# Performance work log

Measured on AMD Instinct MI355X. Metric: run time of the kernel, lower is better.

## Reference

```python
import jax, jax.numpy as jnp
import numpy as np

B, N = 8, 48
NEMBED, EMBED_DIM, HID_DIM = 1000, 32, 32
IN_DIM = EMBED_DIM + 1  # feature dim after concatenating xfeat
N_OPS = 8  # exchangeable 3-tensor basis: identity + means over each nonempty axis subset


def setup_inputs() -> dict:
    key = jax.random.key(0)
    k1, k2, k3, k4, k5 = jax.random.split(key, 5)
    xcat = jax.random.randint(k1, (B, N), 0, NEMBED)
    xfeat = jax.random.normal(k2, (B, N), dtype=jnp.float32)
    embed_table = jax.random.normal(k3, (NEMBED, EMBED_DIM), dtype=jnp.float32)
    # SetEq3to3 coefficients: (in_dim, n_basis_ops, out_dim), Glorot-ish scale
    coefs = jax.random.normal(k4, (IN_DIM, N_OPS, HID_DIM), dtype=jnp.float32) * np.sqrt(2.0 / (IN_DIM + HID_DIM))
    eq_bias = jnp.zeros((HID_DIM,), dtype=jnp.float32)
    out_w = jax.random.normal(k5, (HID_DIM, 1), dtype=jnp.float32) * np.sqrt(1.0 / HID_DIM)
    out_b = jnp.zeros((1,), dtype=jnp.float32)
    return {"xcat": xcat, "xfeat": xfeat, "embed_table": embed_table,
            "coefs": coefs, "eq_bias": eq_bias, "out_w": out_w, "out_b": out_b}


def _set_eq3to3(t, coefs, eq_bias):
    # t: (B, d, n, n, n); coefs: (d, 8, h). Each basis op is a mean over a
    # subset of the three set axes (kept as size-1 dims so broadcasting restores shape).
    def mix(op, s):
        return jnp.einsum('bd...,dh->bh...', op, coefs[:, s, :])
    m_i = t.mean(axis=2, keepdims=True)
    m_j = t.mean(axis=3, keepdims=True)
    m_k = t.mean(axis=4, keepdims=True)
    m_ij = m_i.mean(axis=3, keepdims=True)
    m_ik = m_i.mean(axis=4, keepdims=True)
    m_jk = m_j.mean(axis=4, keepdims=True)
    m_ijk = m_ij.mean(axis=4, keepdims=True)
    out = (mix(t, 0) + mix(m_i, 1) + mix(m_j, 2) + mix(m_k, 3)
           + mix(m_ij, 4) + mix(m_ik, 5) + mix(m_jk, 6) + mix(m_ijk, 7))
    return out + eq_bias.reshape(1, -1, 1, 1, 1)  # (B, h, n, n, n)


def reference(xcat, xfeat, embed_table, coefs, eq_bias, out_w, out_b):
    e = embed_table[xcat]                                   # (B, n, d_e)
    x = jnp.concatenate([e, xfeat[..., None]], axis=-1)      # (B, n, d) with d = d_e + 1
    t = jnp.einsum('bid,bjd,bkd->bdijk', x, x, x)            # (B, d, n, n, n)
    y = _set_eq3to3(t, coefs, eq_bias)                       # (B, h, n, n, n)
    y = jnp.transpose(y, (0, 2, 3, 4, 1))                    # (B, n, n, n, h)
    y = jax.nn.relu(y)
    y = y.mean(axis=(1, 2, 3))                               # (B, h) mean pool
    y = jax.nn.relu(y)
    # dropout is inactive in eval mode (training=False)
    return y @ out_w + out_b                                 # (B, 1)
```

## Files before the change

### kernel.cpp

```cpp
#include <hip/hip_runtime.h>
#include <cstdint>
#include <cstddef>

#define BB 8
#define NN 48
#define DD 33
#define XS 40
#define KP 128
#define HH 32
#define MM (NN*NN)
#define NC (NN*HH)
#define TILE 96
#define TM (MM/TILE)
#define TN (NC/TILE)
#define NBLK (TM*TN)
#define ACHK (MM*16/256)
#define BCHK (NC*16/256)

typedef __attribute__((ext_vector_type(8))) _Float16 f16x8;
typedef __attribute__((ext_vector_type(4))) float f32x4;

__device__ __forceinline__ void gload16(const void* g, void* l) {
    __builtin_amdgcn_global_load_lds(
        (const __attribute__((address_space(1))) unsigned int*)g,
        (__attribute__((address_space(3))) unsigned int*)l, 16, 0, 0);
}

__global__ void k_setup(const int* __restrict__ xcat, const float* __restrict__ xfeat,
                        const float* __restrict__ embed, const float* __restrict__ coefs,
                        const float* __restrict__ eq_bias,
                        float* __restrict__ xw, float* __restrict__ sw,
                        float* __restrict__ ct, float* __restrict__ gk) {
    int b = blockIdx.x, t = threadIdx.x;
    if (b < BB) {
        __shared__ float xl[NN * XS];
        __shared__ float sl[XS];
        __shared__ float c47[2][DD][HH];
        for (int idx = t; idx < 2 * DD * HH; idx += 256) {
            int q = idx / (DD * HH), r = idx - q * DD * HH;
            int d = r >> 5, h = r & 31;
            c47[q][d][h] = coefs[(d * 8 + (q ? 7 : 4)) * HH + h];
        }
        for (int idx = t; idx < NN * XS; idx += 256) {
            int i = idx / XS, d = idx - i * XS;
            float v = 0.f;
            if (d < 32)       v = embed[xcat[b * NN + i] * 32 + d];
            else if (d == 32) v = xfeat[b * NN + i];
            xl[idx] = v;
            xw[b * NN * XS + idx] = v;
        }
        __syncthreads();
        if (t < XS) {
            float a = 0.f;
            for (int i = 0; i < NN; ++i) a += xl[i * XS + t];
            float s = a * (1.0f / 48.0f);
            sw[b * XS + t] = s;
            sl[t] = s;
        }
        __syncthreads();
        for (int idx = t; idx < NC; idx += 256) {
            int k = idx >> 5, h = idx & 31;
            float g = 0.f;
            for (int d = 0; d < DD; ++d) {
                float sd = sl[d];
                g += sd * sd * (c47[0][d][h] * xl[k * XS + d] + c47[1][d][h] * sd);
            }
            gk[b * NC + idx] = g + eq_bias[h];
        }
    } else {
        for (int idx = t; idx < 8 * HH * XS; idx += 256) {
            int qh = idx / XS, d = idx - qh * XS;
            int q = qh >> 5, h = qh & 31;
            ct[idx] = (d < DD) ? coefs[(d * 8 + q) * HH + h] : 0.f;
        }
    }
}

__global__ __launch_bounds__(256) void k_build(
        const float* __restrict__ xw, const float* __restrict__ sw,
        const float* __restrict__ ct, const float* __restrict__ gk,
        _Float16* __restrict__ Aw, _Float16* __restrict__ Bw) {
    int t = threadIdx.x;
    int L = blockIdx.x;
    int b = L & 7;
    int c = L >> 3;
    const float* xb = xw + b * NN * XS;
    const float* sb = sw + b * XS;
    if (c < ACHK) {
        int chunk = c * 256 + t;
        int row = chunk >> 4, d0 = (chunk & 15) * 8;
        int i = row / NN, j = row - i * NN;
        f16x8 v;
        if (d0 < 120) {
            int seg = (d0 >= 80) ? 2 : (d0 >= 40) ? 1 : 0;
            int d = d0 - seg * 40;
            const float* p1 = (seg == 2) ? (xb + j * XS) : (xb + i * XS);
            const float* p2 = (seg == 0) ? (xb + j * XS) : sb;
            f32x4 a0 = *(const f32x4*)(p1 + d), a1 = *(const f32x4*)(p1 + d + 4);
            f32x4 b0 = *(const f32x4*)(p2 + d), b1 = *(const f32x4*)(p2 + d + 4);
            f32x4 r0 = a0 * b0, r1 = a1 * b1;
            for (int e = 0; e < 4; ++e) { v[e] = (_Float16)r0[e]; v[4 + e] = (_Float16)r1[e]; }
        } else {
            v = (f16x8){0, 0, 0, 0, 0, 0, 0, 0};
            v[0] = (_Float16)1.f;
        }
        *(f16x8*)&Aw[((size_t)(b * MM + row)) * KP + d0] = v;
    } else {
        int chunk = (c - ACHK) * 256 + t;
        int row = chunk >> 4, d0 = (chunk & 15) * 8;
        int k = row >> 5, h = row & 31;
        const float* xk = xb + k * XS;
        f16x8 v;
        if (d0 < 120) {
            int seg = (d0 >= 80) ? 2 : (d0 >= 40) ? 1 : 0;
            int d = d0 - seg * 40;
            const int QA[3] = {0, 2, 1}, QB[3] = {3, 6, 5};
            const float* ca = ct + (QA[seg] * HH + h) * XS + d;
            const float* cb = ct + (QB[seg] * HH + h) * XS + d;
            f32x4 ca0 = *(const f32x4*)(ca),     ca1 = *(const f32x4*)(ca + 4);
            f32x4 cb0 = *(const f32x4*)(cb),     cb1 = *(const f32x4*)(cb + 4);
            f32x4 xk0 = *(const f32x4*)(xk + d), xk1 = *(const f32x4*)(xk + d + 4);
            f32x4 sb0 = *(const f32x4*)(sb + d), sb1 = *(const f32x4*)(sb + d + 4);
            f32x4 r0 = ca0 * xk0 + cb0 * sb0;
            f32x4 r1 = ca1 * xk1 + cb1 * sb1;
            for (int e = 0; e < 4; ++e) { v[e] = (_Float16)r0[e]; v[4 + e] = (_Float16)r1[e]; }
        } else {
            v = (f16x8){0, 0, 0, 0, 0, 0, 0, 0};
            v[0] = (_Float16)gk[b * NC + row];
        }
        *(f16x8*)&Bw[((size_t)(b * NC + row)) * KP + d0] = v;
    }
}

__global__ __launch_bounds__(256, 3) void k_gemm(
        const _Float16* __restrict__ Aw, const _Float16* __restrict__ Bw,
        float* __restrict__ partials) {
    __shared__ __align__(16) _Float16 AsF[TILE * KP];
    __shared__ __align__(16) _Float16 BsF[TILE * KP];
    __shared__ float hacc[HH];

    int t = threadIdx.x;
    int lane = t & 63, wave = t >> 6;
    int L = blockIdx.x;
    int b = L & 7;
    int tile = L >> 3;
    int bx = tile & 15, by = tile >> 4;
    int N0 = bx * TILE, M0 = by * TILE;
    const char* Agc = (const char*)(Aw + ((size_t)(b * MM + M0)) * KP);
    const char* Bgc = (const char*)(Bw + ((size_t)(b * NC + N0)) * KP);

    if (t < HH) hacc[t] = 0.f;

#pragma unroll
    for (int c = 0; c < 6; ++c) {
        int row0 = c * 16 + wave * 4;
        int row = row0 + (lane >> 4);
        int src = row * 256 + (((lane & 15) * 16) ^ ((row & 7) << 4));
        gload16(Agc + src, (char*)AsF + row0 * 256);
        gload16(Bgc + src, (char*)BsF + row0 * 256);
    }
    __syncthreads();

    int lrow = lane & 15, quad = lane >> 4;

    f32x4 acc[3][3];
#pragma unroll
    for (int m3 = 0; m3 < 3; ++m3)
#pragma unroll
        for (int nt = 0; nt < 3; ++nt)
            acc[m3][nt] = (f32x4){0.f, 0.f, 0.f, 0.f};

    int wm = (wave >> 1) * 48, wn = (wave & 1) * 48;
#pragma unroll
    for (int ks = 0; ks < 4; ++ks) {
        int cb = ks * 64 + quad * 16;
        f16x8 af[3], bf[3];
#pragma unroll
        for (int m3 = 0; m3 < 3; ++m3) {
            int R = wm + m3 * 16 + lrow;
            af[m3] = *(const f16x8*)((const char*)AsF + R * 256 + (cb ^ ((R & 7) << 4)));
        }
#pragma unroll
        for (int nt = 0; nt < 3; ++nt) {
            int R = wn + nt * 16 + lrow;
            bf[nt] = *(const f16x8*)((const char*)BsF + R * 256 + (cb ^ ((R & 7) << 4)));
        }
#pragma unroll
        for (int m3 = 0; m3 < 3; ++m3)
#pragma unroll
            for (int nt = 0; nt < 3; ++nt)
                acc[m3][nt] = __builtin_amdgcn_mfma_f32_16x16x32_f16(af[m3], bf[nt], acc[m3][nt], 0, 0, 0);
    }

    float fs[3] = {0.f, 0.f, 0.f};
#pragma unroll
    for (int m3 = 0; m3 < 3; ++m3)
#pragma unroll
        for (int nt = 0; nt < 3; ++nt)
#pragma unroll
            for (int r = 0; r < 4; ++r)
                fs[nt] += fmaxf(acc[m3][nt][r], 0.f);

#pragma unroll
    for (int nt = 0; nt < 3; ++nt) {
        float v = fs[nt];
        v += __shfl_xor(v, 16);
        v += __shfl_xor(v, 32);
        if (lane < 16) atomicAdd(&hacc[(wn + nt * 16 + lane) & 31], v);
    }
    __syncthreads();
    if (t < HH) {
        int blockLin = by * TN + bx;
        partials[((size_t)b * NBLK + blockLin) * HH + t] = hacc[t];
    }
}

__global__ void k_final(const float* __restrict__ partials, const float* __restrict__ out_w,
                        const float* __restrict__ out_b, float* __restrict__ out) {
    __shared__ float red[256];
    int b = blockIdx.x, t = threadIdx.x;
    int h = t & 31, g = t >> 5;
    float a = 0.f;
    for (int p = g; p < NBLK; p += 8) a += partials[((size_t)b * NBLK + p) * HH + h];
    red[t] = a;
    __syncthreads();
    if (t < HH) {
        float tot = 0.f;
        for (int gg = 0; gg < 8; ++gg) tot += red[gg * 32 + t];
        float m = tot * (1.0f / 110592.0f);
        red[t] = fmaxf(m, 0.f) * out_w[t];
    }
    __syncthreads();
    if (t == 0) {
        float o = 0.f;
        for (int h2 = 0; h2 < HH; ++h2) o += red[h2];
        out[b] = o + out_b[0];
    }
}

extern "C" void kernel_launch(void* const* d_in, const int* in_sizes, int n_in,
                              void* d_out, int out_size, void* d_ws, size_t ws_size,
                              hipStream_t stream) {
    (void)in_sizes; (void)n_in; (void)out_size; (void)ws_size;
    const int*   xcat    = (const int*)d_in[0];
    const float* xfeat   = (const float*)d_in[1];
    const float* embed   = (const float*)d_in[2];
    const float* coefs   = (const float*)d_in[3];
    const float* eq_bias = (const float*)d_in[4];
    const float* out_w   = (const float*)d_in[5];
    const float* out_b   = (const float*)d_in[6];
    float* out = (float*)d_out;

    char* w = (char*)d_ws;
    float*    xw       = (float*)(w + 0);
    float*    sw       = (float*)(w + 61440);
    float*    ct       = (float*)(w + 62720);
    float*    gk       = (float*)(w + 103680);
    _Float16* Aw       = (_Float16*)(w + 152832);
    _Float16* Bw       = (_Float16*)(w + 4871424);
    float*    partials = (float*)(w + 8017152);

    k_setup<<<dim3(BB + 1), dim3(256), 0, stream>>>(xcat, xfeat, embed, coefs, eq_bias,
                                                    xw, sw, ct, gk);
    k_build<<<dim3((ACHK + BCHK) * BB), dim3(256), 0, stream>>>(xw, sw, ct, gk, Aw, Bw);
    k_gemm<<<dim3(TM * TN * BB), dim3(256), 0, stream>>>(Aw, Bw, partials);
    k_final<<<dim3(BB), dim3(256), 0, stream>>>(partials, out_w, out_b, out);
}
```

Measured before the change: 108.5 us.

## Fuse setup kernel into build kernel, recomputing embeddings and means per block

Removes the separate k_setup launch. Each build block now gathers its batch's embedding rows into LDS and computes the set means itself, and it reads coefs directly instead of the transposed ct copy. The gk bias term is computed inline per row. This saves one kernel launch and the workspace round trip. In exchange, every block redundantly gathers 48x40 values, adds two barriers, does strided scalar coefs loads, and runs a 33-step loop for the bias column.

Result: no change. 106.7 us (-1.7%).

```diff
diff --git a/kernel.cpp b/kernel.cpp
--- a/kernel.cpp
+++ b/kernel.cpp
@@ -26,66 +26,33 @@
         (__attribute__((address_space(3))) unsigned int*)l, 16, 0, 0);
 }
 
-__global__ void k_setup(const int* __restrict__ xcat, const float* __restrict__ xfeat,
-                        const float* __restrict__ embed, const float* __restrict__ coefs,
-                        const float* __restrict__ eq_bias,
-                        float* __restrict__ xw, float* __restrict__ sw,
-                        float* __restrict__ ct, float* __restrict__ gk) {
-    int b = blockIdx.x, t = threadIdx.x;
-    if (b < BB) {
-        __shared__ float xl[NN * XS];
-        __shared__ float sl[XS];
-        __shared__ float c47[2][DD][HH];
-        for (int idx = t; idx < 2 * DD * HH; idx += 256) {
-            int q = idx / (DD * HH), r = idx - q * DD * HH;
-            int d = r >> 5, h = r & 31;
-            c47[q][d][h] = coefs[(d * 8 + (q ? 7 : 4)) * HH + h];
-        }
-        for (int idx = t; idx < NN * XS; idx += 256) {
-            int i = idx / XS, d = idx - i * XS;
-            float v = 0.f;
-            if (d < 32)       v = embed[xcat[b * NN + i] * 32 + d];
-            else if (d == 32) v = xfeat[b * NN + i];
-            xl[idx] = v;
-            xw[b * NN * XS + idx] = v;
-        }
-        __syncthreads();
-        if (t < XS) {
-            float a = 0.f;
-            for (int i = 0; i < NN; ++i) a += xl[i * XS + t];
-            float s = a * (1.0f / 48.0f);
-            sw[b * XS + t] = s;
-            sl[t] = s;
-        }
-        __syncthreads();
-        for (int idx = t; idx < NC; idx += 256) {
-            int k = idx >> 5, h = idx & 31;
-            float g = 0.f;
-            for (int d = 0; d < DD; ++d) {
-                float sd = sl[d];
-                g += sd * sd * (c47[0][d][h] * xl[k * XS + d] + c47[1][d][h] * sd);
-            }
-            gk[b * NC + idx] = g + eq_bias[h];
-        }
-    } else {
-        for (int idx = t; idx < 8 * HH * XS; idx += 256) {
-            int qh = idx / XS, d = idx - qh * XS;
-            int q = qh >> 5, h = qh & 31;
-            ct[idx] = (d < DD) ? coefs[(d * 8 + q) * HH + h] : 0.f;
-        }
-    }
-}
-
 __global__ __launch_bounds__(256) void k_build(
-        const float* __restrict__ xw, const float* __restrict__ sw,
-        const float* __restrict__ ct, const float* __restrict__ gk,
+        const int* __restrict__ xcat, const float* __restrict__ xfeat,
+        const float* __restrict__ embed, const float* __restrict__ coefs,
+        const float* __restrict__ eq_bias,
         _Float16* __restrict__ Aw, _Float16* __restrict__ Bw) {
+    __shared__ float xl[NN * XS];
+    __shared__ float sl[XS];
     int t = threadIdx.x;
     int L = blockIdx.x;
     int b = L & 7;
     int c = L >> 3;
-    const float* xb = xw + b * NN * XS;
-    const float* sb = sw + b * XS;
+
+    for (int idx = t; idx < NN * XS; idx += 256) {
+        int i = idx / XS, d = idx - i * XS;
+        float v = 0.f;
+        if (d < 32)       v = embed[xcat[b * NN + i] * 32 + d];
+        else if (d == 32) v = xfeat[b * NN + i];
+        xl[idx] = v;
+    }
+    __syncthreads();
+    if (t < XS) {
+        float a = 0.f;
+        for (int i = 0; i < NN; ++i) a += xl[i * XS + t];
+        sl[t] = a * (1.0f / 48.0f);
+    }
+    __syncthreads();
+
     if (c < ACHK) {
         int chunk = c * 256 + t;
         int row = chunk >> 4, d0 = (chunk & 15) * 8;
@@ -94,8 +61,8 @@
         if (d0 < 120) {
             int seg = (d0 >= 80) ? 2 : (d0 >= 40) ? 1 : 0;
             int d = d0 - seg * 40;
-            const float* p1 = (seg == 2) ? (xb + j * XS) : (xb + i * XS);
-            const float* p2 = (seg == 0) ? (xb + j * XS) : sb;
+            const float* p1 = (seg == 2) ? (xl + j * XS) : (xl + i * XS);
+            const float* p2 = (seg == 0) ? (xl + j * XS) : sl;
             f32x4 a0 = *(const f32x4*)(p1 + d), a1 = *(const f32x4*)(p1 + d + 4);
             f32x4 b0 = *(const f32x4*)(p2 + d), b1 = *(const f32x4*)(p2 + d + 4);
             f32x4 r0 = a0 * b0, r1 = a1 * b1;
@@ -109,24 +76,28 @@
         int chunk = (c - ACHK) * 256 + t;
         int row = chunk >> 4, d0 = (chunk & 15) * 8;
         int k = row >> 5, h = row & 31;
-        const float* xk = xb + k * XS;
         f16x8 v;
         if (d0 < 120) {
             int seg = (d0 >= 80) ? 2 : (d0 >= 40) ? 1 : 0;
             int d = d0 - seg * 40;
             const int QA[3] = {0, 2, 1}, QB[3] = {3, 6, 5};
-            const float* ca = ct + (QA[seg] * HH + h) * XS + d;
-            const float* cb = ct + (QB[seg] * HH + h) * XS + d;
-            f32x4 ca0 = *(const f32x4*)(ca),     ca1 = *(const f32x4*)(ca + 4);
-            f32x4 cb0 = *(const f32x4*)(cb),     cb1 = *(const f32x4*)(cb + 4);
-            f32x4 xk0 = *(const f32x4*)(xk + d), xk1 = *(const f32x4*)(xk + d + 4);
-            f32x4 sb0 = *(const f32x4*)(sb + d), sb1 = *(const f32x4*)(sb + d + 4);
-            f32x4 r0 = ca0 * xk0 + cb0 * sb0;
-            f32x4 r1 = ca1 * xk1 + cb1 * sb1;
-            for (int e = 0; e < 4; ++e) { v[e] = (_Float16)r0[e]; v[4 + e] = (_Float16)r1[e]; }
+            int qa = QA[seg], qb = QB[seg];
+#pragma unroll
+            for (int e = 0; e < 8; ++e) {
+                int dd = d + e;
+                float ca = (dd < DD) ? coefs[(dd * 8 + qa) * HH + h] : 0.f;
+                float cb = (dd < DD) ? coefs[(dd * 8 + qb) * HH + h] : 0.f;
+                v[e] = (_Float16)(ca * xl[k * XS + dd] + cb * sl[dd]);
+            }
         } else {
+            float g = 0.f;
+            for (int d = 0; d < DD; ++d) {
+                float sd = sl[d];
+                g += sd * sd * (coefs[(d * 8 + 4) * HH + h] * xl[k * XS + d]
+                              + coefs[(d * 8 + 7) * HH + h] * sd);
+            }
             v = (f16x8){0, 0, 0, 0, 0, 0, 0, 0};
-            v[0] = (_Float16)gk[b * NC + row];
+            v[0] = (_Float16)(g + eq_bias[h]);
         }
         *(f16x8*)&Bw[((size_t)(b * NC + row)) * KP + d0] = v;
     }
@@ -252,17 +223,12 @@
     float* out = (float*)d_out;
 
     char* w = (char*)d_ws;
-    float*    xw       = (float*)(w + 0);
-    float*    sw       = (float*)(w + 61440);
-    float*    ct       = (float*)(w + 62720);
-    float*    gk       = (float*)(w + 103680);
-    _Float16* Aw       = (_Float16*)(w + 152832);
-    _Float16* Bw       = (_Float16*)(w + 4871424);
-    float*    partials = (float*)(w + 8017152);
-
-    k_setup<<<dim3(BB + 1), dim3(256), 0, stream>>>(xcat, xfeat, embed, coefs, eq_bias,
-                                                    xw, sw, ct, gk);
-    k_build<<<dim3((ACHK + BCHK) * BB), dim3(256), 0, stream>>>(xw, sw, ct, gk, Aw, Bw);
+    _Float16* Aw       = (_Float16*)(w + 0);
+    _Float16* Bw       = (_Float16*)(w + 4718592);
+    float*    partials = (float*)(w + 7864320);
+
+    k_build<<<dim3((ACHK + BCHK) * BB), dim3(256), 0, stream>>>(xcat, xfeat, embed, coefs,
+                                                                eq_bias, Aw, Bw);
     k_gemm<<<dim3(TM * TN * BB), dim3(256), 0, stream>>>(Aw, Bw, partials);
     k_final<<<dim3(BB), dim3(256), 0, stream>>>(partials, out_w, out_b, out);
 }
```
